# Performance work log

Measured on AMD Instinct MI355X. Metric: run time of the kernel, lower is better.

## Reference

```python
import jax, jax.numpy as jnp
import numpy as np

NUM_LEVELS = 4
NUM_CODES = 1024
EMBED_DIM = 256
B, T = 16, 2048


def setup_inputs() -> dict:
    key = jax.random.key(0)
    k1, k2 = jax.random.split(key)
    x = jax.random.normal(k1, (B, T, EMBED_DIM), dtype=jnp.float32)
    # original init: uniform(-1/num_codes, 1/num_codes)
    u = jax.random.uniform(k2, (NUM_LEVELS, NUM_CODES, EMBED_DIM), dtype=jnp.float32)
    codebooks = (u * 2.0 - 1.0) / NUM_CODES
    return {"x": x, "codebooks": codebooks}


def _vq_level(residual_flat, cb):
    # residual_flat: [N, D], cb: [K, D]
    # squared L2 distances: ||r||^2 + ||c||^2 - 2 r.c  -> [N, K]
    dists = (
        jnp.sum(residual_flat ** 2, axis=1, keepdims=True)
        + jnp.sum(cb ** 2, axis=1)
        - 2.0 * residual_flat @ cb.T
    )
    idx = jnp.argmin(dists, axis=1)  # [N]
    quant = cb[idx]  # [N, D] gather
    return quant, idx


def reference(x, codebooks):
    sg = jax.lax.stop_gradient
    shape = x.shape
    D = shape[-1]
    L = codebooks.shape[0]
    residual = x
    total_quant = jnp.zeros_like(x)
    total_q_loss = jnp.float32(0.0)
    total_e_loss = jnp.float32(0.0)
    all_indices = []
    for lvl in range(L):
        flat = residual.reshape(-1, D)
        quant_flat, idx = _vq_level(flat, codebooks[lvl])
        quant = quant_flat.reshape(shape)
        total_q_loss = total_q_loss + jnp.mean((quant - sg(residual)) ** 2)
        total_e_loss = total_e_loss + jnp.mean((sg(quant) - residual) ** 2)
        total_quant = total_quant + quant
        all_indices.append(idx.reshape(shape[:-1]))
        residual = residual - sg(quant)
    quantized_ste = x + sg(total_quant - x)
    q_loss = total_q_loss / L
    e_loss = total_e_loss / L
    indices = jnp.stack(all_indices, axis=0)  # [L, B, T]
    return quantized_ste, q_loss, e_loss, indices
```

## Files before the change

### kernel.cpp

```cpp
#include <hip/hip_runtime.h>

#define NROWS 32768
#define DIM 256
#define KCODES 1024
#define NLEV 4
#define CAP 64
#define MARGIN 8e-3f

typedef short short8v __attribute__((ext_vector_type(8)));
typedef float f32x4v  __attribute__((ext_vector_type(4)));

static __device__ __forceinline__ unsigned short f2bf(float f) {
  unsigned u = __float_as_uint(f);
  unsigned lsb = (u >> 16) & 1u;
  u += 0x7fffu + lsb;
  return (unsigned short)(u >> 16);
}


__global__ __launch_bounds__(256) void k_bnorm(const float* __restrict__ cb,
                                               float* __restrict__ bv) {
  int r = blockIdx.x * blockDim.x + threadIdx.x;
  if (r >= NLEV * KCODES) return;
  const float4* p = reinterpret_cast<const float4*>(cb + (size_t)r * DIM);
  float s0 = 0.f, s1 = 0.f, s2 = 0.f, s3 = 0.f;
  for (int g = 0; g < DIM / 4; ++g) {
    float4 v = p[g];
    s0 += v.x * v.x; s1 += v.y * v.y; s2 += v.z * v.z; s3 += v.w * v.w;
  }
  bv[r] = (s0 + s1) + (s2 + s3);
}

__global__ __launch_bounds__(256) void k_csplit(const float* __restrict__ cb,
                                                unsigned short* __restrict__ chi) {
  const int tid = threadIdx.x;
  const int cr = blockIdx.x * 16 + (tid >> 4);
  const int l16 = tid & 15;
  const float4* p = reinterpret_cast<const float4*>(cb + (size_t)cr * DIM + l16 * 16);
  unsigned w[8];
  #pragma unroll
  for (int j = 0; j < 4; ++j) {
    float4 v = p[j];
    w[2 * j + 0] = (unsigned)f2bf(v.x) | ((unsigned)f2bf(v.y) << 16);
    w[2 * j + 1] = (unsigned)f2bf(v.z) | ((unsigned)f2bf(v.w) << 16);
  }
  const int lvl_ = cr >> 10;
  const int c = cr & 1023;
  unsigned short* base = chi + (size_t)lvl_ * (KCODES * DIM) + (size_t)(c >> 4) * 4096;
  const int c8 = c & 15;
  const int ks = l16 >> 1;
  const int kb0 = (l16 & 1) * 2;
  *reinterpret_cast<uint4*>(base + ks * 512 + kb0 * 128 + c8 * 8) =
      make_uint4(w[0], w[1], w[2], w[3]);
  *reinterpret_cast<uint4*>(base + ks * 512 + (kb0 + 1) * 128 + c8 * 8) =
      make_uint4(w[4], w[5], w[6], w[7]);
}

__global__ __launch_bounds__(256) void k_prep(const float* __restrict__ x,
                                              unsigned short* __restrict__ rhi,
                                              float* __restrict__ rowsq) {
  __shared__ float sred[256];
  const int tid = threadIdx.x;
  const int rr = tid >> 4;
  const int l16 = tid & 15;
  const int row = blockIdx.x * 16 + rr;
  const float4* p = reinterpret_cast<const float4*>(x + (size_t)row * DIM + l16 * 16);
  float e = 0.f;
  unsigned w[8];
  #pragma unroll
  for (int j = 0; j < 4; ++j) {
    float4 v = p[j];
    e += v.x * v.x + v.y * v.y + v.z * v.z + v.w * v.w;
    w[2 * j + 0] = (unsigned)f2bf(v.x) | ((unsigned)f2bf(v.y) << 16);
    w[2 * j + 1] = (unsigned)f2bf(v.z) | ((unsigned)f2bf(v.w) << 16);
  }
  unsigned short* base = rhi + (size_t)blockIdx.x * 4096;
  const int ks = l16 >> 1;
  const int kb0 = (l16 & 1) * 2;
  *reinterpret_cast<uint4*>(base + ks * 512 + kb0 * 128 + rr * 8) =
      make_uint4(w[0], w[1], w[2], w[3]);
  *reinterpret_cast<uint4*>(base + ks * 512 + (kb0 + 1) * 128 + rr * 8) =
      make_uint4(w[4], w[5], w[6], w[7]);
  sred[tid] = e;
  __syncthreads();
  if (tid < 16) {
    float s = 0.f;
    #pragma unroll
    for (int k = 0; k < 16; ++k) s += sred[tid * 16 + k];
    rowsq[blockIdx.x * 16 + tid] = s;
  }
}

__global__ __launch_bounds__(512, 4) void k_screen(const unsigned short* __restrict__ rhi,
                                                   const unsigned short* __restrict__ chi_l,
                                                   const float* __restrict__ bv_l,
                                                   const float* __restrict__ rowsq,
                                                   unsigned* __restrict__ survq,
                                                   unsigned* __restrict__ counts) {
  __shared__ float minb[32][8];
  __shared__ float rowminf[32];
  __shared__ unsigned cnt[32];
  const int tid = threadIdx.x;
  const int lane = tid & 63;
  const int w = tid >> 6;
  const int rb = blockIdx.x;
  const int row0 = rb * 32;
  const int c0 = w * 128;
  const int ln = lane & 15;
  const int kb = lane >> 4;

  f32x4v acc[2][8];
  #pragma unroll
  for (int r = 0; r < 2; ++r)
    #pragma unroll
    for (int t = 0; t < 8; ++t) acc[r][t] = (f32x4v){0.f, 0.f, 0.f, 0.f};

  const unsigned short* pa = rhi + (size_t)(rb * 2) * 4096 + lane * 8;
  const unsigned short* pb = chi_l + (size_t)(w * 8) * 4096 + lane * 8;

  #pragma unroll
  for (int ks = 0; ks < 8; ++ks) {
    short8v a0 = *reinterpret_cast<const short8v*>(pa + ks * 512);
    short8v a1 = *reinterpret_cast<const short8v*>(pa + 4096 + ks * 512);
    short8v b0 = *reinterpret_cast<const short8v*>(pb + 0 * 4096 + ks * 512);
    short8v b1 = *reinterpret_cast<const short8v*>(pb + 1 * 4096 + ks * 512);
    short8v b2 = *reinterpret_cast<const short8v*>(pb + 2 * 4096 + ks * 512);
    short8v b3 = *reinterpret_cast<const short8v*>(pb + 3 * 4096 + ks * 512);
    short8v b4 = *reinterpret_cast<const short8v*>(pb + 4 * 4096 + ks * 512);
    short8v b5 = *reinterpret_cast<const short8v*>(pb + 5 * 4096 + ks * 512);
    short8v b6 = *reinterpret_cast<const short8v*>(pb + 6 * 4096 + ks * 512);
    short8v b7 = *reinterpret_cast<const short8v*>(pb + 7 * 4096 + ks * 512);
    __builtin_amdgcn_sched_barrier(0);
    acc[0][0] = __builtin_amdgcn_mfma_f32_16x16x32_bf16(a0, b0, acc[0][0], 0, 0, 0);
    acc[1][0] = __builtin_amdgcn_mfma_f32_16x16x32_bf16(a1, b0, acc[1][0], 0, 0, 0);
    acc[0][1] = __builtin_amdgcn_mfma_f32_16x16x32_bf16(a0, b1, acc[0][1], 0, 0, 0);
    acc[1][1] = __builtin_amdgcn_mfma_f32_16x16x32_bf16(a1, b1, acc[1][1], 0, 0, 0);
    acc[0][2] = __builtin_amdgcn_mfma_f32_16x16x32_bf16(a0, b2, acc[0][2], 0, 0, 0);
    acc[1][2] = __builtin_amdgcn_mfma_f32_16x16x32_bf16(a1, b2, acc[1][2], 0, 0, 0);
    acc[0][3] = __builtin_amdgcn_mfma_f32_16x16x32_bf16(a0, b3, acc[0][3], 0, 0, 0);
    acc[1][3] = __builtin_amdgcn_mfma_f32_16x16x32_bf16(a1, b3, acc[1][3], 0, 0, 0);
    acc[0][4] = __builtin_amdgcn_mfma_f32_16x16x32_bf16(a0, b4, acc[0][4], 0, 0, 0);
    acc[1][4] = __builtin_amdgcn_mfma_f32_16x16x32_bf16(a1, b4, acc[1][4], 0, 0, 0);
    acc[0][5] = __builtin_amdgcn_mfma_f32_16x16x32_bf16(a0, b5, acc[0][5], 0, 0, 0);
    acc[1][5] = __builtin_amdgcn_mfma_f32_16x16x32_bf16(a1, b5, acc[1][5], 0, 0, 0);
    acc[0][6] = __builtin_amdgcn_mfma_f32_16x16x32_bf16(a0, b6, acc[0][6], 0, 0, 0);
    acc[1][6] = __builtin_amdgcn_mfma_f32_16x16x32_bf16(a1, b6, acc[1][6], 0, 0, 0);
    acc[0][7] = __builtin_amdgcn_mfma_f32_16x16x32_bf16(a0, b7, acc[0][7], 0, 0, 0);
    acc[1][7] = __builtin_amdgcn_mfma_f32_16x16x32_bf16(a1, b7, acc[1][7], 0, 0, 0);
  }

  float bvl[8];
  #pragma unroll
  for (int t = 0; t < 8; ++t) bvl[t] = bv_l[c0 + t * 16 + ln];
  float rq[2][4];
  #pragma unroll
  for (int r = 0; r < 2; ++r)
    #pragma unroll
    for (int g = 0; g < 4; ++g) rq[r][g] = rowsq[row0 + r * 16 + kb * 4 + g];

  #pragma unroll
  for (int r = 0; r < 2; ++r) {
    #pragma unroll
    for (int g = 0; g < 4; ++g) {
      float v = __builtin_inff();
      #pragma unroll
      for (int t = 0; t < 8; ++t) {
        float dd = (rq[r][g] + bvl[t]) - 2.0f * acc[r][t][g];
        v = fminf(v, dd);
      }
      #pragma unroll
      for (int m = 1; m < 16; m <<= 1) v = fminf(v, __shfl_xor(v, m));
      if (ln == 0) minb[r * 16 + kb * 4 + g][w] = v;
    }
  }
  __syncthreads();
  if (tid < 32) {
    float v = minb[tid][0];
    #pragma unroll
    for (int k = 1; k < 8; ++k) v = fminf(v, minb[tid][k]);
    rowminf[tid] = v;
    cnt[tid] = 0;
  }
  __syncthreads();
  #pragma unroll
  for (int r = 0; r < 2; ++r) {
    #pragma unroll
    for (int g = 0; g < 4; ++g) {
      const int rowloc = r * 16 + kb * 4 + g;
      const float thr = rowminf[rowloc] + MARGIN;
      #pragma unroll
      for (int t = 0; t < 8; ++t) {
        float dd = (rq[r][g] + bvl[t]) - 2.0f * acc[r][t][g];
        if (dd <= thr) {
          unsigned slot = atomicAdd(&cnt[rowloc], 1u);
          if (slot < CAP)
            survq[(size_t)(row0 + rowloc) * CAP + slot] =
                (unsigned)(c0 + t * 16 + ln);
        }
      }
    }
  }
  __syncthreads();
  if (tid < 32) counts[row0 + tid] = cnt[tid];
}

__global__ __launch_bounds__(256) void k_exupd(const float* __restrict__ x,
                                               const float* __restrict__ cb,
                                               const float* __restrict__ bv,
                                               const float* __restrict__ rowsq,
                                               const unsigned* __restrict__ survq,
                                               const unsigned* __restrict__ counts,
                                               int* __restrict__ idxh,
                                               float* __restrict__ fidx,
                                               float* __restrict__ tq,
                                               float* __restrict__ part,
                                               float* __restrict__ rowsq_o,
                                               unsigned short* __restrict__ rhi,
                                               int lvl) {
  __shared__ __align__(16) float rlds[16][260];
  __shared__ int idsh[16];
  __shared__ float sred[256];
  __shared__ float rsum[16];

  const int tid = threadIdx.x;
  const int rr = tid >> 4;
  const int l16 = tid & 15;
  const int row = blockIdx.x * 16 + rr;
  const size_t obase = (size_t)row * DIM + l16 * 16;
  const float* cb_l = cb + (size_t)lvl * KCODES * DIM;
  const float* bv_l = bv + lvl * KCODES;

  float4 xj[4], rj[4];
  {
    const float4* xp = reinterpret_cast<const float4*>(x + obase);
    #pragma unroll
    for (int j = 0; j < 4; ++j) { xj[j] = xp[j]; rj[j] = xj[j]; }
    for (int p = 0; p < lvl; ++p) {
      const float4* qp = reinterpret_cast<const float4*>(
          cb + ((size_t)p * KCODES + idxh[p * NROWS + row]) * DIM + l16 * 16);
      #pragma unroll
      for (int j = 0; j < 4; ++j) {
        float4 q = qp[j];
        rj[j].x -= q.x; rj[j].y -= q.y; rj[j].z -= q.z; rj[j].w -= q.w;
      }
    }
    #pragma unroll
    for (int j = 0; j < 4; ++j)
      *reinterpret_cast<float4*>(&rlds[rr][l16 * 16 + 4 * j]) = rj[j];
  }
  __syncthreads();

  const float A = rowsq[row];
  const unsigned n = counts[row];
  unsigned long long best = ~0ull;

#define CHAIN(CODE)                                                            \
  {                                                                            \
    const float* cp2 = cb_l + (size_t)(CODE) * DIM;                            \
    float a0 = 0.f;                                                            \
    _Pragma("unroll 8")                                                        \
    for (int dv = 0; dv < DIM / 4; ++dv) {                                     \
      float4 rv = *reinterpret_cast<const float4*>(&rlds[rr][dv * 4]);         \
      float4 cv = *reinterpret_cast<const float4*>(cp2 + dv * 4);              \
      a0 = fmaf(rv.x, cv.x, a0); a0 = fmaf(rv.y, cv.y, a0);                    \
      a0 = fmaf(rv.z, cv.z, a0); a0 = fmaf(rv.w, cv.w, a0);                    \
    }                                                                          \
    float t = A + bv_l[(CODE)];                                 \
    float dd = t - 2.0f * a0;                  \
    unsigned long long pk =                                                    \
        ((unsigned long long)__float_as_uint(dd) << 32) | (unsigned)(CODE);    \
    best = (pk < best) ? pk : best;                                            \
  }

  if (n <= CAP) {
    for (unsigned s = l16; s < n; s += 16) {
      unsigned code = survq[(size_t)row * CAP + s];
      CHAIN(code);
    }
  } else {
    for (unsigned c = l16; c < KCODES; c += 16) CHAIN(c);
  }
#undef CHAIN

  #pragma unroll
  for (int m = 1; m < 16; m <<= 1) {
    unsigned long long o = __shfl_xor(best, m);
    best = (o < best) ? o : best;
  }
  if (l16 == 0) {
    const int id = (int)(best & 0xffffffffull);
    idxh[lvl * NROWS + row] = id;
    fidx[lvl * NROWS + row] = (float)id;
    idsh[rr] = id;
  }
  __syncthreads();

  const int id = idsh[rr];
  const float4* cpc = reinterpret_cast<const float4*>(
      cb_l + (size_t)id * DIM + l16 * 16);
  float4* tp = reinterpret_cast<float4*>(tq + obase);
  float nn[16];
  float e = 0.f;
  #pragma unroll
  for (int j = 0; j < 4; ++j) {
    float4 c = cpc[j];
    float n0 = rj[j].x - c.x, n1 = rj[j].y - c.y;
    float n2 = rj[j].z - c.z, n3 = rj[j].w - c.w;
    nn[4 * j + 0] = n0; nn[4 * j + 1] = n1; nn[4 * j + 2] = n2; nn[4 * j + 3] = n3;
    e += (n0 * n0 + n1 * n1) + (n2 * n2 + n3 * n3);
    float4 tv;
    if (lvl == 0) {
      tv = c;
    } else {
      tv = tp[j];
      tv.x += c.x; tv.y += c.y; tv.z += c.z; tv.w += c.w;
    }
    if (lvl == 3) {
      tv.x = xj[j].x + (tv.x - xj[j].x); tv.y = xj[j].y + (tv.y - xj[j].y);
      tv.z = xj[j].z + (tv.z - xj[j].z); tv.w = xj[j].w + (tv.w - xj[j].w);
    }
    tp[j] = tv;
  }

  if (lvl < 3) {
    unsigned w[8];
    #pragma unroll
    for (int k = 0; k < 8; ++k)
      w[k] = (unsigned)f2bf(nn[2 * k]) | ((unsigned)f2bf(nn[2 * k + 1]) << 16);
    unsigned short* base = rhi + (size_t)blockIdx.x * 4096;
    const int ks = l16 >> 1;
    const int kb0 = (l16 & 1) * 2;
    *reinterpret_cast<uint4*>(base + ks * 512 + kb0 * 128 + rr * 8) =
        make_uint4(w[0], w[1], w[2], w[3]);
    *reinterpret_cast<uint4*>(base + ks * 512 + (kb0 + 1) * 128 + rr * 8) =
        make_uint4(w[4], w[5], w[6], w[7]);
  }

  sred[tid] = e;
  __syncthreads();
  if (tid < 16) {
    float s = 0.f;
    #pragma unroll
    for (int k = 0; k < 16; ++k) s += sred[tid * 16 + k];
    rsum[tid] = s;
    if (lvl < 3) rowsq_o[blockIdx.x * 16 + tid] = s;
  }
  __syncthreads();
  if (tid == 0) {
    float p = 0.f;
    #pragma unroll
    for (int k = 0; k < 16; ++k) p += rsum[k];
    part[blockIdx.x] = p;
  }
}

__global__ __launch_bounds__(256) void k_loss(const float* __restrict__ part,
                                              float* __restrict__ out) {
  __shared__ float s[256];
  const int tid = threadIdx.x;
  float means[4];
  for (int l = 0; l < 4; ++l) {
    float sum = 0.f;
    for (int i = tid; i < 2048; i += 256) sum += part[l * 2048 + i];
    s[tid] = sum;
    __syncthreads();
    for (int st = 128; st > 0; st >>= 1) {
      if (tid < st) s[tid] += s[tid + st];
      __syncthreads();
    }
    means[l] = s[0] * (1.0f / 8388608.0f);
    __syncthreads();
  }
  if (tid == 0) {
    float t = ((means[0] + means[1]) + means[2]) + means[3];
    float loss = t * 0.25f;
    out[0] = loss;
    out[1] = loss;
  }
}

extern "C" void kernel_launch(void* const* d_in, const int* in_sizes, int n_in,
                              void* d_out, int out_size, void* d_ws, size_t ws_size,
                              hipStream_t stream) {
  const float* x  = (const float*)d_in[0];
  const float* cb = (const float*)d_in[1];
  float* out = (float*)d_out;
  float* ws  = (float*)d_ws;

  unsigned short* rhi = (unsigned short*)ws;
  unsigned short* chi = (unsigned short*)(ws + 4194304);
  unsigned* survq  = (unsigned*)(ws + 4194304 + 524288);
  unsigned* counts = (unsigned*)(ws + 4194304 + 524288 + 2097152);
  int* idxh = (int*)(ws + 4194304 + 524288 + 2097152 + 131072);
  float* bv    = ws + 4194304 + 524288 + 2097152 + 131072 + 131072;
  float* rowsq = bv + 4096;
  float* part  = rowsq + 32768;

  float* tq      = out;
  float* lossout = out + 8388608;
  float* fidx    = out + 8388610;

  k_bnorm<<<16, 256, 0, stream>>>(cb, bv);
  k_csplit<<<256, 256, 0, stream>>>(cb, chi);
  k_prep<<<2048, 256, 0, stream>>>(x, rhi, rowsq);

  for (int l = 0; l < NLEV; ++l) {
    k_screen<<<1024, 512, 0, stream>>>(rhi, chi + (size_t)l * KCODES * DIM,
                                       bv + l * KCODES, rowsq, survq, counts);
    k_exupd<<<2048, 256, 0, stream>>>(x, cb, bv, rowsq, survq, counts,
                                      idxh, fidx, tq, part + l * 2048,
                                      rowsq, rhi, l);
  }

  k_loss<<<1, 256, 0, stream>>>(part, lossout);
}
```

Measured before the change: 426.4 us.

## Double-buffer operand loads in screen kernel and relax occupancy bound

The screen kernel's K loop now uses two register sets of A/B fragments. The next k-step's global loads are issued before the current step's MFMAs run, so load latency overlaps with compute. The launch bound drops from 4 to 2 blocks per CU to make room for the extra registers. This trades occupancy for software prefetch, and the loop is no longer fully unrolled.

```diff
diff --git a/kernel.cpp b/kernel.cpp
--- a/kernel.cpp
+++ b/kernel.cpp
@@ -91,7 +91,7 @@
   }
 }
 
-__global__ __launch_bounds__(512, 4) void k_screen(const unsigned short* __restrict__ rhi,
+__global__ __launch_bounds__(512, 2) void k_screen(const unsigned short* __restrict__ rhi,
                                                    const unsigned short* __restrict__ chi_l,
                                                    const float* __restrict__ bv_l,
                                                    const float* __restrict__ rowsq,
@@ -118,36 +118,53 @@
   const unsigned short* pa = rhi + (size_t)(rb * 2) * 4096 + lane * 8;
   const unsigned short* pb = chi_l + (size_t)(w * 8) * 4096 + lane * 8;
 
-  #pragma unroll
-  for (int ks = 0; ks < 8; ++ks) {
-    short8v a0 = *reinterpret_cast<const short8v*>(pa + ks * 512);
-    short8v a1 = *reinterpret_cast<const short8v*>(pa + 4096 + ks * 512);
-    short8v b0 = *reinterpret_cast<const short8v*>(pb + 0 * 4096 + ks * 512);
-    short8v b1 = *reinterpret_cast<const short8v*>(pb + 1 * 4096 + ks * 512);
-    short8v b2 = *reinterpret_cast<const short8v*>(pb + 2 * 4096 + ks * 512);
-    short8v b3 = *reinterpret_cast<const short8v*>(pb + 3 * 4096 + ks * 512);
-    short8v b4 = *reinterpret_cast<const short8v*>(pb + 4 * 4096 + ks * 512);
-    short8v b5 = *reinterpret_cast<const short8v*>(pb + 5 * 4096 + ks * 512);
-    short8v b6 = *reinterpret_cast<const short8v*>(pb + 6 * 4096 + ks * 512);
-    short8v b7 = *reinterpret_cast<const short8v*>(pb + 7 * 4096 + ks * 512);
+  short8v aA0, aA1, bA0, bA1, bA2, bA3, bA4, bA5, bA6, bA7;
+  short8v aB0, aB1, bB0, bB1, bB2, bB3, bB4, bB5, bB6, bB7;
+
+#define LOADSET(A0, A1, B0, B1, B2, B3, B4, B5, B6, B7, KS)                    \
+  A0 = *reinterpret_cast<const short8v*>(pa + (KS) * 512);                     \
+  A1 = *reinterpret_cast<const short8v*>(pa + 4096 + (KS) * 512);              \
+  B0 = *reinterpret_cast<const short8v*>(pb + 0 * 4096 + (KS) * 512);          \
+  B1 = *reinterpret_cast<const short8v*>(pb + 1 * 4096 + (KS) * 512);          \
+  B2 = *reinterpret_cast<const short8v*>(pb + 2 * 4096 + (KS) * 512);          \
+  B3 = *reinterpret_cast<const short8v*>(pb + 3 * 4096 + (KS) * 512);          \
+  B4 = *reinterpret_cast<const short8v*>(pb + 4 * 4096 + (KS) * 512);          \
+  B5 = *reinterpret_cast<const short8v*>(pb + 5 * 4096 + (KS) * 512);          \
+  B6 = *reinterpret_cast<const short8v*>(pb + 6 * 4096 + (KS) * 512);          \
+  B7 = *reinterpret_cast<const short8v*>(pb + 7 * 4096 + (KS) * 512);
+
+#define MFMASET(A0, A1, B0, B1, B2, B3, B4, B5, B6, B7)                        \
+  acc[0][0] = __builtin_amdgcn_mfma_f32_16x16x32_bf16(A0, B0, acc[0][0], 0, 0, 0); \
+  acc[1][0] = __builtin_amdgcn_mfma_f32_16x16x32_bf16(A1, B0, acc[1][0], 0, 0, 0); \
+  acc[0][1] = __builtin_amdgcn_mfma_f32_16x16x32_bf16(A0, B1, acc[0][1], 0, 0, 0); \
+  acc[1][1] = __builtin_amdgcn_mfma_f32_16x16x32_bf16(A1, B1, acc[1][1], 0, 0, 0); \
+  acc[0][2] = __builtin_amdgcn_mfma_f32_16x16x32_bf16(A0, B2, acc[0][2], 0, 0, 0); \
+  acc[1][2] = __builtin_amdgcn_mfma_f32_16x16x32_bf16(A1, B2, acc[1][2], 0, 0, 0); \
+  acc[0][3] = __builtin_amdgcn_mfma_f32_16x16x32_bf16(A0, B3, acc[0][3], 0, 0, 0); \
+  acc[1][3] = __builtin_amdgcn_mfma_f32_16x16x32_bf16(A1, B3, acc[1][3], 0, 0, 0); \
+  acc[0][4] = __builtin_amdgcn_mfma_f32_16x16x32_bf16(A0, B4, acc[0][4], 0, 0, 0); \
+  acc[1][4] = __builtin_amdgcn_mfma_f32_16x16x32_bf16(A1, B4, acc[1][4], 0, 0, 0); \
+  acc[0][5] = __builtin_amdgcn_mfma_f32_16x16x32_bf16(A0, B5, acc[0][5], 0, 0, 0); \
+  acc[1][5] = __builtin_amdgcn_mfma_f32_16x16x32_bf16(A1, B5, acc[1][5], 0, 0, 0); \
+  acc[0][6] = __builtin_amdgcn_mfma_f32_16x16x32_bf16(A0, B6, acc[0][6], 0, 0, 0); \
+  acc[1][6] = __builtin_amdgcn_mfma_f32_16x16x32_bf16(A1, B6, acc[1][6], 0, 0, 0); \
+  acc[0][7] = __builtin_amdgcn_mfma_f32_16x16x32_bf16(A0, B7, acc[0][7], 0, 0, 0); \
+  acc[1][7] = __builtin_amdgcn_mfma_f32_16x16x32_bf16(A1, B7, acc[1][7], 0, 0, 0);
+
+  LOADSET(aA0, aA1, bA0, bA1, bA2, bA3, bA4, bA5, bA6, bA7, 0)
+  #pragma unroll 1
+  for (int i = 0; i < 4; ++i) {
+    LOADSET(aB0, aB1, bB0, bB1, bB2, bB3, bB4, bB5, bB6, bB7, 2 * i + 1)
     __builtin_amdgcn_sched_barrier(0);
-    acc[0][0] = __builtin_amdgcn_mfma_f32_16x16x32_bf16(a0, b0, acc[0][0], 0, 0, 0);
-    acc[1][0] = __builtin_amdgcn_mfma_f32_16x16x32_bf16(a1, b0, acc[1][0], 0, 0, 0);
-    acc[0][1] = __builtin_amdgcn_mfma_f32_16x16x32_bf16(a0, b1, acc[0][1], 0, 0, 0);
-    acc[1][1] = __builtin_amdgcn_mfma_f32_16x16x32_bf16(a1, b1, acc[1][1], 0, 0, 0);
-    acc[0][2] = __builtin_amdgcn_mfma_f32_16x16x32_bf16(a0, b2, acc[0][2], 0, 0, 0);
-    acc[1][2] = __builtin_amdgcn_mfma_f32_16x16x32_bf16(a1, b2, acc[1][2], 0, 0, 0);
-    acc[0][3] = __builtin_amdgcn_mfma_f32_16x16x32_bf16(a0, b3, acc[0][3], 0, 0, 0);
-    acc[1][3] = __builtin_amdgcn_mfma_f32_16x16x32_bf16(a1, b3, acc[1][3], 0, 0, 0);
-    acc[0][4] = __builtin_amdgcn_mfma_f32_16x16x32_bf16(a0, b4, acc[0][4], 0, 0, 0);
-    acc[1][4] = __builtin_amdgcn_mfma_f32_16x16x32_bf16(a1, b4, acc[1][4], 0, 0, 0);
-    acc[0][5] = __builtin_amdgcn_mfma_f32_16x16x32_bf16(a0, b5, acc[0][5], 0, 0, 0);
-    acc[1][5] = __builtin_amdgcn_mfma_f32_16x16x32_bf16(a1, b5, acc[1][5], 0, 0, 0);
-    acc[0][6] = __builtin_amdgcn_mfma_f32_16x16x32_bf16(a0, b6, acc[0][6], 0, 0, 0);
-    acc[1][6] = __builtin_amdgcn_mfma_f32_16x16x32_bf16(a1, b6, acc[1][6], 0, 0, 0);
-    acc[0][7] = __builtin_amdgcn_mfma_f32_16x16x32_bf16(a0, b7, acc[0][7], 0, 0, 0);
-    acc[1][7] = __builtin_amdgcn_mfma_f32_16x16x32_bf16(a1, b7, acc[1][7], 0, 0, 0);
-  }
+    MFMASET(aA0, aA1, bA0, bA1, bA2, bA3, bA4, bA5, bA6, bA7)
+    if (i < 3) {
+      LOADSET(aA0, aA1, bA0, bA1, bA2, bA3, bA4, bA5, bA6, bA7, 2 * i + 2)
+    }
+    __builtin_amdgcn_sched_barrier(0);
+    MFMASET(aB0, aB1, bB0, bB1, bB2, bB3, bB4, bB5, bB6, bB7)
+  }
+#undef LOADSET
+#undef MFMASET
 
   float bvl[8];
   #pragma unroll
```

Measured after the change: 418.5 us. No clear change (-1.9%).
